# Kernel optimization log

Measured on AMD Instinct MI355X. Metric: run time of the kernel, lower is better.

Reference implementation:

```python
import jax, jax.numpy as jnp
import numpy as np

N = 50000      # nodes
E = 800000     # edges
XS = 64        # x_size
ES = 32        # edge_attr dim (in_size = XS + ES = 96)
OUT = 64       # out_size
H = 128        # hidden_size
EPS = 1e-5


def _lin_init(k, fan_in, fan_out):
    s = 1.0 / np.sqrt(fan_in)
    kw, kb = jax.random.split(k)
    w = jax.random.uniform(kw, (fan_in, fan_out), minval=-s, maxval=s, dtype=jnp.float32)
    b = jax.random.uniform(kb, (fan_out,), minval=-s, maxval=s, dtype=jnp.float32)
    return w, b


def setup_inputs() -> dict:
    key = jax.random.key(0)
    ks = jax.random.split(key, 12)
    x = jax.random.normal(ks[0], (N, XS), dtype=jnp.float32)
    edge_index = jax.random.randint(ks[1], (2, E), 0, N, dtype=jnp.int64)
    edge_attr = jax.random.normal(ks[2], (E, ES), dtype=jnp.float32)
    u = jax.random.normal(ks[3], (1, 8), dtype=jnp.float32)
    batch = jnp.zeros((N,), dtype=jnp.int64)
    # MLP1: (96->128) LReLU (128->128) LReLU (128->64) LReLU LN(64)
    m1w0, m1b0 = _lin_init(ks[4], XS + ES, H)
    m1w1, m1b1 = _lin_init(ks[5], H, H)
    m1w2, m1b2 = _lin_init(ks[6], H, OUT)
    ln1_g = jnp.ones((OUT,), jnp.float32); ln1_b = jnp.zeros((OUT,), jnp.float32)
    # MLP2: (128->128) LReLU (128->128) LReLU (128->64) LReLU LN(64)
    m2w0, m2b0 = _lin_init(ks[7], XS + OUT, H)
    m2w1, m2b1 = _lin_init(ks[8], H, H)
    m2w2, m2b2 = _lin_init(ks[9], H, OUT)
    ln2_g = jnp.ones((OUT,), jnp.float32); ln2_b = jnp.zeros((OUT,), jnp.float32)
    return dict(x=x, edge_index=edge_index, edge_attr=edge_attr, u=u, batch=batch,
                m1w0=m1w0, m1b0=m1b0, m1w1=m1w1, m1b1=m1b1, m1w2=m1w2, m1b2=m1b2,
                ln1_g=ln1_g, ln1_b=ln1_b,
                m2w0=m2w0, m2b0=m2b0, m2w1=m2w1, m2b1=m2b1, m2w2=m2w2, m2b2=m2b2,
                ln2_g=ln2_g, ln2_b=ln2_b)


def _lrelu(v):
    return jax.nn.leaky_relu(v, 0.01)


def _layernorm(v, g, b):
    mu = jnp.mean(v, axis=-1, keepdims=True)
    var = jnp.mean(jnp.square(v - mu), axis=-1, keepdims=True)
    return (v - mu) * jax.lax.rsqrt(var + EPS) * g + b


def _mlp(h, w0, b0, w1, b1, w2, b2, g, bn):
    h = _lrelu(h @ w0 + b0)
    h = _lrelu(h @ w1 + b1)
    h = _lrelu(h @ w2 + b2)          # activate_last=True
    return _layernorm(h, g, bn)      # layer_norm=True


def reference(x, edge_index, edge_attr, u, batch,
              m1w0, m1b0, m1w1, m1b1, m1w2, m1b2, ln1_g, ln1_b,
              m2w0, m2b0, m2w1, m2b1, m2w2, m2b2, ln2_g, ln2_b):
    row, col = edge_index[0], edge_index[1]
    # gather source nodes, concat edge features -> per-edge MLP
    h = jnp.concatenate([x[row], edge_attr], axis=1)            # [E, 96]
    h = _mlp(h, m1w0, m1b0, m1w1, m1b1, m1w2, m1b2, ln1_g, ln1_b)  # [E, 64]
    # scatter_mean over destination nodes
    agg = jax.ops.segment_sum(h, col, num_segments=N)           # [N, 64]
    cnt = jax.ops.segment_sum(jnp.ones((E,), h.dtype), col, num_segments=N)
    agg = agg / jnp.maximum(cnt, 1.0)[:, None]
    # node update MLP
    h2 = jnp.concatenate([x, agg], axis=1)                      # [N, 128]
    return _mlp(h2, m2w0, m2b0, m2w1, m2b1, m2w2, m2b2, ln2_g, ln2_b)
```

## Files before the change

### kernel.cpp

```cpp
#include <hip/hip_runtime.h>


#define NNODES 50000
#define NEDGES 800000

typedef __bf16 bf16;
typedef __bf16 __attribute__((ext_vector_type(4))) bf16x4;
typedef __bf16 __attribute__((ext_vector_type(8))) bf16x8;
typedef float __attribute__((ext_vector_type(4))) f32x4;

__device__ __forceinline__ f32x4 mfma_bf16(bf16x8 a, bf16x8 b, f32x4 c) {
    return __builtin_amdgcn_mfma_f32_16x16x32_bf16(a, b, c, 0, 0, 0);
}

__global__ void prep_weights(const float* __restrict__ w10, const float* __restrict__ w11,
                             const float* __restrict__ w12, const float* __restrict__ w20,
                             const float* __restrict__ w21, const float* __restrict__ w22,
                             bf16* __restrict__ img) {
    int idx = blockIdx.x * 256 + threadIdx.x;
    if (idx >= 77824) return;
    const float* w; int N; int t;
    if (idx < 12288)      { w = w10; N = 128; t = idx; }
    else if (idx < 28672) { w = w11; N = 128; t = idx - 12288; }
    else if (idx < 36864) { w = w12; N = 64;  t = idx - 28672; }
    else if (idx < 53248) { w = w20; N = 128; t = idx - 36864; }
    else if (idx < 69632) { w = w21; N = 128; t = idx - 53248; }
    else                  { w = w22; N = 64;  t = idx - 69632; }
    int j = t & 7, lane = (t >> 3) & 63, blk = t >> 9;
    int NT = N >> 4;
    int nt = blk % NT, ks = blk / NT;
    int k = ks * 32 + ((lane >> 4) << 3) + j;
    int n = nt * 16 + (lane & 15);
    img[idx] = (bf16)w[k * N + n];
}

__global__ void hist_kernel(const int* __restrict__ col, int* __restrict__ hist) {
    int i = blockIdx.x * 512 + threadIdx.x;
    if (i < NEDGES) atomicAdd(hist + col[i], 1);
}

__global__ void scanA(const int* __restrict__ hist, int* __restrict__ off,
                      int* __restrict__ csum) {
    __shared__ int sd[512];
    int t = threadIdx.x, i = blockIdx.x * 512 + t;
    int v = (i < NNODES) ? hist[i] : 0;
    sd[t] = v;
    __syncthreads();
    for (int o2 = 1; o2 < 512; o2 <<= 1) {
        int x = (t >= o2) ? sd[t - o2] : 0;
        __syncthreads();
        sd[t] += x;
        __syncthreads();
    }
    if (i < NNODES) off[i] = sd[t] - v;
    if (t == 511) csum[blockIdx.x] = sd[511];
}

__global__ void scanB(int* __restrict__ csum) {
    __shared__ int sd[128];
    int t = threadIdx.x;
    int v = (t < 98) ? csum[t] : 0;
    sd[t] = v;
    __syncthreads();
    for (int o2 = 1; o2 < 128; o2 <<= 1) {
        int x = (t >= o2) ? sd[t - o2] : 0;
        __syncthreads();
        sd[t] += x;
        __syncthreads();
    }
    if (t < 98) csum[t] = sd[t] - v;
}

__global__ void scanC(int* __restrict__ off, const int* __restrict__ csum) {
    int i = blockIdx.x * 512 + threadIdx.x;
    if (i < NNODES) off[i] += csum[blockIdx.x];
}

__global__ void scatter_kernel(const int* __restrict__ eidx, int* __restrict__ off,
                               int2* __restrict__ prd) {
    int i = blockIdx.x * 512 + threadIdx.x;
    if (i < NEDGES) {
        int r = eidx[i], d = eidx[NEDGES + i];
        int pos = atomicAdd(off + d, 1);
        prd[pos] = make_int2(i, r | (d << 16));
    }
}

__global__ __launch_bounds__(256, 2) void edge_mlp(
    const float* __restrict__ x, const int2* __restrict__ prd,
    const float* __restrict__ eattr, const bf16* __restrict__ wimg,
    const float* __restrict__ b0g, const float* __restrict__ b1g,
    const float* __restrict__ b2g, const float* __restrict__ lng,
    const float* __restrict__ lnb, float* __restrict__ agg) {
    __shared__ __align__(16) bf16 atile[128 * 104];
    __shared__ __align__(16) bf16 hid[128 * 136];

    const int tid = threadIdx.x;
    const int lane = tid & 63;
    const int wv = tid >> 6;
    const int col16 = lane & 15;
    const int quad = lane >> 4;

    float b0r[8], b1r[8], b2r[4], gr[4], br[4];
#pragma unroll
    for (int i = 0; i < 8; i++) { b0r[i] = b0g[i * 16 + col16]; b1r[i] = b1g[i * 16 + col16]; }
#pragma unroll
    for (int i = 0; i < 4; i++) {
        b2r[i] = b2g[i * 16 + col16];
        gr[i] = lng[i * 16 + col16];
        br[i] = lnb[i * 16 + col16];
    }

    const bf16* wl = wimg + (size_t)lane * 8;
    const f32x4 vzero = {0.0f, 0.0f, 0.0f, 0.0f};
    const int r0 = wv * 32 + col16;
    const int rw = wv * 32 + quad * 4;
    const int sbase = blockIdx.x * 128;

    int vreg;
    {
        const int el = tid >> 1, half = tid & 1;
        int2 v = prd[sbase + el];
        vreg = v.y;
        const int r = v.y & 0xFFFF;
        const float4* xs = (const float4*)(x + (size_t)r * 64);
        bf16* arow = atile + el * 104;
#pragma unroll
        for (int j = 0; j < 8; j++) {
            float4 vv = xs[half * 8 + j];
            bf16x4 u = {(bf16)vv.x, (bf16)vv.y, (bf16)vv.z, (bf16)vv.w};
            *(bf16x4*)(arow + half * 32 + j * 4) = u;
        }
        const float4* es = (const float4*)(eattr + (size_t)v.x * 32);
#pragma unroll
        for (int j = 0; j < 4; j++) {
            float4 vv = es[half * 4 + j];
            bf16x4 u = {(bf16)vv.x, (bf16)vv.y, (bf16)vv.z, (bf16)vv.w};
            *(bf16x4*)(arow + 64 + half * 16 + j * 4) = u;
        }
    }

    f32x4 acc1[2][8];
#pragma unroll
    for (int mt = 0; mt < 2; mt++)
#pragma unroll
        for (int nt = 0; nt < 8; nt++) acc1[mt][nt] = vzero;
#pragma unroll
    for (int ks = 0; ks < 3; ks++) {
        bf16x8 a0 = *(const bf16x8*)(atile + r0 * 104 + ks * 32 + quad * 8);
        bf16x8 a1 = *(const bf16x8*)(atile + (r0 + 16) * 104 + ks * 32 + quad * 8);
#pragma unroll
        for (int nt = 0; nt < 8; nt++) {
            bf16x8 b = *(const bf16x8*)(wl + (ks * 8 + nt) * 512);
            acc1[0][nt] = mfma_bf16(a0, b, acc1[0][nt]);
            acc1[1][nt] = mfma_bf16(a1, b, acc1[1][nt]);
        }
    }
#pragma unroll
    for (int mt = 0; mt < 2; mt++)
#pragma unroll
        for (int nt = 0; nt < 8; nt++)
#pragma unroll
            for (int rg = 0; rg < 4; rg++) {
                float v = acc1[mt][nt][rg] + b0r[nt];
                v = (v > 0.0f) ? v : 0.01f * v;
                hid[(rw + mt * 16 + rg) * 136 + nt * 16 + col16] = (bf16)v;
            }

    bf16x8 a2[2][4];
#pragma unroll
    for (int mt = 0; mt < 2; mt++)
#pragma unroll
        for (int ks = 0; ks < 4; ks++)
            a2[mt][ks] = *(const bf16x8*)(hid + (r0 + mt * 16) * 136 + ks * 32 + quad * 8);
    f32x4 acc2[2][8];
#pragma unroll
    for (int mt = 0; mt < 2; mt++)
#pragma unroll
        for (int nt = 0; nt < 8; nt++) acc2[mt][nt] = vzero;
#pragma unroll
    for (int ks = 0; ks < 4; ks++) {
#pragma unroll
        for (int nt = 0; nt < 8; nt++) {
            bf16x8 b = *(const bf16x8*)(wl + 12288 + (ks * 8 + nt) * 512);
            acc2[0][nt] = mfma_bf16(a2[0][ks], b, acc2[0][nt]);
            acc2[1][nt] = mfma_bf16(a2[1][ks], b, acc2[1][nt]);
        }
    }
#pragma unroll
    for (int mt = 0; mt < 2; mt++)
#pragma unroll
        for (int nt = 0; nt < 8; nt++)
#pragma unroll
            for (int rg = 0; rg < 4; rg++) {
                float v = acc2[mt][nt][rg] + b1r[nt];
                v = (v > 0.0f) ? v : 0.01f * v;
                hid[(rw + mt * 16 + rg) * 136 + nt * 16 + col16] = (bf16)v;
            }

    bf16x8 a3[2][4];
#pragma unroll
    for (int mt = 0; mt < 2; mt++)
#pragma unroll
        for (int ks = 0; ks < 4; ks++)
            a3[mt][ks] = *(const bf16x8*)(hid + (r0 + mt * 16) * 136 + ks * 32 + quad * 8);
    f32x4 acc3[2][4];
#pragma unroll
    for (int mt = 0; mt < 2; mt++)
#pragma unroll
        for (int nt = 0; nt < 4; nt++) acc3[mt][nt] = vzero;
#pragma unroll
    for (int ks = 0; ks < 4; ks++) {
#pragma unroll
        for (int nt = 0; nt < 4; nt++) {
            bf16x8 b = *(const bf16x8*)(wl + 28672 + (ks * 4 + nt) * 512);
            acc3[0][nt] = mfma_bf16(a3[0][ks], b, acc3[0][nt]);
            acc3[1][nt] = mfma_bf16(a3[1][ks], b, acc3[1][nt]);
        }
    }

#pragma unroll
    for (int mt = 0; mt < 2; mt++) {
        float vals[4][4];
        float s1[4] = {0.f, 0.f, 0.f, 0.f}, s2[4] = {0.f, 0.f, 0.f, 0.f};
#pragma unroll
        for (int nt = 0; nt < 4; nt++)
#pragma unroll
            for (int rg = 0; rg < 4; rg++) {
                float v = acc3[mt][nt][rg] + b2r[nt];
                v = (v > 0.0f) ? v : 0.01f * v;
                vals[nt][rg] = v;
                s1[rg] += v;
                s2[rg] += v * v;
            }
#pragma unroll
        for (int off2 = 1; off2 < 16; off2 <<= 1) {
#pragma unroll
            for (int rg = 0; rg < 4; rg++) {
                s1[rg] += __shfl_xor(s1[rg], off2);
                s2[rg] += __shfl_xor(s2[rg], off2);
            }
        }
        float o[4][4];
        int dr[4];
#pragma unroll
        for (int rg = 0; rg < 4; rg++) {
            float mu = s1[rg] * 0.015625f;
            float var = s2[rg] * 0.015625f - mu * mu;
            float rstd = rsqrtf(var + 1e-5f);
            dr[rg] = ((unsigned)__shfl(vreg, (mt * 16 + quad * 4 + rg) << 1)) >> 16;
#pragma unroll
            for (int nt = 0; nt < 4; nt++)
                o[nt][rg] = (vals[nt][rg] - mu) * rstd * gr[nt] + br[nt];
        }
        float run0 = o[0][0], run1 = o[1][0], run2 = o[2][0], run3 = o[3][0];
        int cur = dr[0];
#pragma unroll
        for (int rg = 1; rg < 4; rg++) {
            if (dr[rg] != cur) {
                float* dst = agg + (size_t)cur * 64 + col16;
                atomicAdd(dst, run0); atomicAdd(dst + 16, run1);
                atomicAdd(dst + 32, run2); atomicAdd(dst + 48, run3);
                run0 = o[0][rg]; run1 = o[1][rg]; run2 = o[2][rg]; run3 = o[3][rg];
                cur = dr[rg];
            } else {
                run0 += o[0][rg]; run1 += o[1][rg]; run2 += o[2][rg]; run3 += o[3][rg];
            }
        }
        float* dst = agg + (size_t)cur * 64 + col16;
        atomicAdd(dst, run0); atomicAdd(dst + 16, run1);
        atomicAdd(dst + 32, run2); atomicAdd(dst + 48, run3);
    }
}

__global__ __launch_bounds__(256, 2) void node_mlp(
    const float* __restrict__ x, const float* __restrict__ agg,
    const int* __restrict__ hist, const bf16* __restrict__ wimg,
    const float* __restrict__ b0g, const float* __restrict__ b1g,
    const float* __restrict__ b2g, const float* __restrict__ lng,
    const float* __restrict__ lnb, float* __restrict__ out) {
    __shared__ __align__(16) bf16 atile[128 * 136];
    __shared__ __align__(16) bf16 hid[128 * 136];

    const int tid = threadIdx.x;
    const int lane = tid & 63;
    const int wv = tid >> 6;
    const int col16 = lane & 15;
    const int quad = lane >> 4;

    float b0r[8], b1r[8], b2r[4], gr[4], br[4];
#pragma unroll
    for (int i = 0; i < 8; i++) { b0r[i] = b0g[i * 16 + col16]; b1r[i] = b1g[i * 16 + col16]; }
#pragma unroll
    for (int i = 0; i < 4; i++) {
        b2r[i] = b2g[i * 16 + col16];
        gr[i] = lng[i * 16 + col16];
        br[i] = lnb[i * 16 + col16];
    }

    const bf16* wl = wimg + 36864 + (size_t)lane * 8;
    const f32x4 vzero = {0.0f, 0.0f, 0.0f, 0.0f};
    const int r0 = wv * 32 + col16;
    const int rw = wv * 32 + quad * 4;
    const int nbase = blockIdx.x * 128;

    {
        const int el = tid >> 1, half = tid & 1;
        int i = nbase + el;
        if (i >= NNODES) i = NNODES - 1;
        const float4* xs = (const float4*)(x + (size_t)i * 64);
        bf16* arow = atile + el * 136;
#pragma unroll
        for (int j = 0; j < 8; j++) {
            float4 v = xs[half * 8 + j];
            bf16x4 u = {(bf16)v.x, (bf16)v.y, (bf16)v.z, (bf16)v.w};
            *(bf16x4*)(arow + half * 32 + j * 4) = u;
        }
        int c = hist[i];
        float inv = 1.0f / (float)(c > 1 ? c : 1);
        const float4* as = (const float4*)(agg + (size_t)i * 64);
#pragma unroll
        for (int j = 0; j < 8; j++) {
            float4 v = as[half * 8 + j];
            bf16x4 u = {(bf16)(v.x * inv), (bf16)(v.y * inv), (bf16)(v.z * inv), (bf16)(v.w * inv)};
            *(bf16x4*)(arow + 64 + half * 32 + j * 4) = u;
        }
    }

    f32x4 acc1[2][8];
#pragma unroll
    for (int mt = 0; mt < 2; mt++)
#pragma unroll
        for (int nt = 0; nt < 8; nt++) acc1[mt][nt] = vzero;
#pragma unroll
    for (int ks = 0; ks < 4; ks++) {
        bf16x8 a0 = *(const bf16x8*)(atile + r0 * 136 + ks * 32 + quad * 8);
        bf16x8 a1 = *(const bf16x8*)(atile + (r0 + 16) * 136 + ks * 32 + quad * 8);
#pragma unroll
        for (int nt = 0; nt < 8; nt++) {
            bf16x8 b = *(const bf16x8*)(wl + (ks * 8 + nt) * 512);
            acc1[0][nt] = mfma_bf16(a0, b, acc1[0][nt]);
            acc1[1][nt] = mfma_bf16(a1, b, acc1[1][nt]);
        }
    }
#pragma unroll
    for (int mt = 0; mt < 2; mt++)
#pragma unroll
        for (int nt = 0; nt < 8; nt++)
#pragma unroll
            for (int rg = 0; rg < 4; rg++) {
                float v = acc1[mt][nt][rg] + b0r[nt];
                v = (v > 0.0f) ? v : 0.01f * v;
                hid[(rw + mt * 16 + rg) * 136 + nt * 16 + col16] = (bf16)v;
            }

    bf16x8 a2[2][4];
#pragma unroll
    for (int mt = 0; mt < 2; mt++)
#pragma unroll
        for (int ks = 0; ks < 4; ks++)
            a2[mt][ks] = *(const bf16x8*)(hid + (r0 + mt * 16) * 136 + ks * 32 + quad * 8);
    f32x4 acc2[2][8];
#pragma unroll
    for (int mt = 0; mt < 2; mt++)
#pragma unroll
        for (int nt = 0; nt < 8; nt++) acc2[mt][nt] = vzero;
#pragma unroll
    for (int ks = 0; ks < 4; ks++) {
#pragma unroll
        for (int nt = 0; nt < 8; nt++) {
            bf16x8 b = *(const bf16x8*)(wl + 16384 + (ks * 8 + nt) * 512);
            acc2[0][nt] = mfma_bf16(a2[0][ks], b, acc2[0][nt]);
            acc2[1][nt] = mfma_bf16(a2[1][ks], b, acc2[1][nt]);
        }
    }
#pragma unroll
    for (int mt = 0; mt < 2; mt++)
#pragma unroll
        for (int nt = 0; nt < 8; nt++)
#pragma unroll
            for (int rg = 0; rg < 4; rg++) {
                float v = acc2[mt][nt][rg] + b1r[nt];
                v = (v > 0.0f) ? v : 0.01f * v;
                hid[(rw + mt * 16 + rg) * 136 + nt * 16 + col16] = (bf16)v;
            }

    bf16x8 a3[2][4];
#pragma unroll
    for (int mt = 0; mt < 2; mt++)
#pragma unroll
        for (int ks = 0; ks < 4; ks++)
            a3[mt][ks] = *(const bf16x8*)(hid + (r0 + mt * 16) * 136 + ks * 32 + quad * 8);
    f32x4 acc3[2][4];
#pragma unroll
    for (int mt = 0; mt < 2; mt++)
#pragma unroll
        for (int nt = 0; nt < 4; nt++) acc3[mt][nt] = vzero;
#pragma unroll
    for (int ks = 0; ks < 4; ks++) {
#pragma unroll
        for (int nt = 0; nt < 4; nt++) {
            bf16x8 b = *(const bf16x8*)(wl + 32768 + (ks * 4 + nt) * 512);
            acc3[0][nt] = mfma_bf16(a3[0][ks], b, acc3[0][nt]);
            acc3[1][nt] = mfma_bf16(a3[1][ks], b, acc3[1][nt]);
        }
    }

#pragma unroll
    for (int mt = 0; mt < 2; mt++) {
        float vals[4][4];
        float s1[4] = {0.f, 0.f, 0.f, 0.f}, s2[4] = {0.f, 0.f, 0.f, 0.f};
#pragma unroll
        for (int nt = 0; nt < 4; nt++)
#pragma unroll
            for (int rg = 0; rg < 4; rg++) {
                float v = acc3[mt][nt][rg] + b2r[nt];
                v = (v > 0.0f) ? v : 0.01f * v;
                vals[nt][rg] = v;
                s1[rg] += v;
                s2[rg] += v * v;
            }
#pragma unroll
        for (int off2 = 1; off2 < 16; off2 <<= 1) {
#pragma unroll
            for (int rg = 0; rg < 4; rg++) {
                s1[rg] += __shfl_xor(s1[rg], off2);
                s2[rg] += __shfl_xor(s2[rg], off2);
            }
        }
#pragma unroll
        for (int rg = 0; rg < 4; rg++) {
            float mu = s1[rg] * 0.015625f;
            float var = s2[rg] * 0.015625f - mu * mu;
            float rstd = rsqrtf(var + 1e-5f);
            int i = nbase + rw + mt * 16 + rg;
            if (i < NNODES) {
#pragma unroll
                for (int nt = 0; nt < 4; nt++) {
                    float o = (vals[nt][rg] - mu) * rstd * gr[nt] + br[nt];
                    out[(size_t)i * 64 + nt * 16 + col16] = o;
                }
            }
        }
    }
}

extern "C" void kernel_launch(void* const* d_in, const int* in_sizes, int n_in,
                              void* d_out, int out_size, void* d_ws, size_t ws_size,
                              hipStream_t stream) {
    (void)in_sizes; (void)n_in; (void)out_size; (void)ws_size;
    const float* x     = (const float*)d_in[0];
    const int*   eidx  = (const int*)d_in[1];
    const float* eattr = (const float*)d_in[2];
    const float* m1w0 = (const float*)d_in[5];
    const float* m1b0 = (const float*)d_in[6];
    const float* m1w1 = (const float*)d_in[7];
    const float* m1b1 = (const float*)d_in[8];
    const float* m1w2 = (const float*)d_in[9];
    const float* m1b2 = (const float*)d_in[10];
    const float* ln1g = (const float*)d_in[11];
    const float* ln1b = (const float*)d_in[12];
    const float* m2w0 = (const float*)d_in[13];
    const float* m2b0 = (const float*)d_in[14];
    const float* m2w1 = (const float*)d_in[15];
    const float* m2b1 = (const float*)d_in[16];
    const float* m2w2 = (const float*)d_in[17];
    const float* m2b2 = (const float*)d_in[18];
    const float* ln2g = (const float*)d_in[19];
    const float* ln2b = (const float*)d_in[20];

    char* ws = (char*)d_ws;
    float* agg  = (float*)ws;
    int*   hist = (int*)(ws + 12800000);
    int*   off  = (int*)(ws + 13000000);
    int*   csum = (int*)(ws + 13200000);
    int2*  prd  = (int2*)(ws + 13200512);
    bf16*  wimg = (bf16*)(ws + 19600512);

    hipMemsetAsync(d_ws, 0, 13000000, stream);
    prep_weights<<<304, 256, 0, stream>>>(m1w0, m1w1, m1w2, m2w0, m2w1, m2w2, wimg);
    hist_kernel<<<1563, 512, 0, stream>>>(eidx + NEDGES, hist);
    scanA<<<98, 512, 0, stream>>>(hist, off, csum);
    scanB<<<1, 128, 0, stream>>>(csum);
    scanC<<<98, 512, 0, stream>>>(off, csum);
    scatter_kernel<<<1563, 512, 0, stream>>>(eidx, off, prd);
    edge_mlp<<<6250, 256, 0, stream>>>(x, prd, eattr, wimg, m1b0, m1b1, m1b2,
                                       ln1g, ln1b, agg);
    node_mlp<<<391, 256, 0, stream>>>(x, agg, hist, wimg,
                                      m2b0, m2b1, m2b2, ln2g, ln2b, (float*)d_out);
}
```

Before: 558.9 us.

## Fold scan fixup into scatter and shrink node MLP blocks to one wave

Drops the separate scanC kernel launch. The scatter kernel now adds the per-block scan prefix (csum[d>>9]) itself when it computes each edge's slot. The node MLP is restructured from 256-thread, 128-row blocks to single-wave, 32-row blocks. Each lane loads its x and agg fragments straight into MFMA A-operand registers instead of staging them through a shared tile. This removes one launch, cuts shared memory, and spreads the node stage over more blocks, at the cost of extra csum reads in the scatter and more weight fetches per node row.

```diff
diff --git a/kernel.cpp b/kernel.cpp
--- a/kernel.cpp
+++ b/kernel.cpp
@@ -11,6 +11,13 @@
 
 __device__ __forceinline__ f32x4 mfma_bf16(bf16x8 a, bf16x8 b, f32x4 c) {
     return __builtin_amdgcn_mfma_f32_16x16x32_bf16(a, b, c, 0, 0, 0);
+}
+
+__device__ __forceinline__ bf16x8 pack8(float4 a, float4 b) {
+    bf16x8 r;
+    r[0] = (bf16)a.x; r[1] = (bf16)a.y; r[2] = (bf16)a.z; r[3] = (bf16)a.w;
+    r[4] = (bf16)b.x; r[5] = (bf16)b.y; r[6] = (bf16)b.z; r[7] = (bf16)b.w;
+    return r;
 }
 
 __global__ void prep_weights(const float* __restrict__ w10, const float* __restrict__ w11,
@@ -71,17 +78,12 @@
     if (t < 98) csum[t] = sd[t] - v;
 }
 
-__global__ void scanC(int* __restrict__ off, const int* __restrict__ csum) {
-    int i = blockIdx.x * 512 + threadIdx.x;
-    if (i < NNODES) off[i] += csum[blockIdx.x];
-}
-
 __global__ void scatter_kernel(const int* __restrict__ eidx, int* __restrict__ off,
-                               int2* __restrict__ prd) {
+                               const int* __restrict__ csum, int2* __restrict__ prd) {
     int i = blockIdx.x * 512 + threadIdx.x;
     if (i < NEDGES) {
         int r = eidx[i], d = eidx[NEDGES + i];
-        int pos = atomicAdd(off + d, 1);
+        int pos = atomicAdd(off + d, 1) + csum[d >> 9];
         prd[pos] = make_int2(i, r | (d << 16));
     }
 }
@@ -273,18 +275,15 @@
     }
 }
 
-__global__ __launch_bounds__(256, 2) void node_mlp(
+__global__ __launch_bounds__(64, 4) void node_mlp(
     const float* __restrict__ x, const float* __restrict__ agg,
     const int* __restrict__ hist, const bf16* __restrict__ wimg,
     const float* __restrict__ b0g, const float* __restrict__ b1g,
     const float* __restrict__ b2g, const float* __restrict__ lng,
     const float* __restrict__ lnb, float* __restrict__ out) {
-    __shared__ __align__(16) bf16 atile[128 * 136];
-    __shared__ __align__(16) bf16 hid[128 * 136];
-
-    const int tid = threadIdx.x;
-    const int lane = tid & 63;
-    const int wv = tid >> 6;
+    __shared__ __align__(16) bf16 hid[32 * 136];
+
+    const int lane = threadIdx.x;
     const int col16 = lane & 15;
     const int quad = lane >> 4;
 
@@ -300,31 +299,29 @@
 
     const bf16* wl = wimg + 36864 + (size_t)lane * 8;
     const f32x4 vzero = {0.0f, 0.0f, 0.0f, 0.0f};
-    const int r0 = wv * 32 + col16;
-    const int rw = wv * 32 + quad * 4;
-    const int nbase = blockIdx.x * 128;
-
-    {
-        const int el = tid >> 1, half = tid & 1;
-        int i = nbase + el;
+    const int nbase = blockIdx.x * 32;
+
+    bf16x8 a1[2][4];
+#pragma unroll
+    for (int mt = 0; mt < 2; mt++) {
+        int i = nbase + col16 + 16 * mt;
         if (i >= NNODES) i = NNODES - 1;
-        const float4* xs = (const float4*)(x + (size_t)i * 64);
-        bf16* arow = atile + el * 136;
-#pragma unroll
-        for (int j = 0; j < 8; j++) {
-            float4 v = xs[half * 8 + j];
-            bf16x4 u = {(bf16)v.x, (bf16)v.y, (bf16)v.z, (bf16)v.w};
-            *(bf16x4*)(arow + half * 32 + j * 4) = u;
-        }
+        const float4* xr = (const float4*)(x + (size_t)i * 64);
+        float4 x0 = xr[quad * 2], x1 = xr[quad * 2 + 1];
+        float4 x2 = xr[8 + quad * 2], x3 = xr[8 + quad * 2 + 1];
         int c = hist[i];
         float inv = 1.0f / (float)(c > 1 ? c : 1);
-        const float4* as = (const float4*)(agg + (size_t)i * 64);
-#pragma unroll
-        for (int j = 0; j < 8; j++) {
-            float4 v = as[half * 8 + j];
-            bf16x4 u = {(bf16)(v.x * inv), (bf16)(v.y * inv), (bf16)(v.z * inv), (bf16)(v.w * inv)};
-            *(bf16x4*)(arow + 64 + half * 32 + j * 4) = u;
-        }
+        const float4* ar = (const float4*)(agg + (size_t)i * 64);
+        float4 g0 = ar[quad * 2], g1 = ar[quad * 2 + 1];
+        float4 g2 = ar[8 + quad * 2], g3 = ar[8 + quad * 2 + 1];
+        a1[mt][0] = pack8(x0, x1);
+        a1[mt][1] = pack8(x2, x3);
+        float4 h0 = {g0.x * inv, g0.y * inv, g0.z * inv, g0.w * inv};
+        float4 h1 = {g1.x * inv, g1.y * inv, g1.z * inv, g1.w * inv};
+        float4 h2 = {g2.x * inv, g2.y * inv, g2.z * inv, g2.w * inv};
+        float4 h3 = {g3.x * inv, g3.y * inv, g3.z * inv, g3.w * inv};
+        a1[mt][2] = pack8(h0, h1);
+        a1[mt][3] = pack8(h2, h3);
     }
 
     f32x4 acc1[2][8];
@@ -334,15 +331,14 @@
         for (int nt = 0; nt < 8; nt++) acc1[mt][nt] = vzero;
 #pragma unroll
     for (int ks = 0; ks < 4; ks++) {
-        bf16x8 a0 = *(const bf16x8*)(atile + r0 * 136 + ks * 32 + quad * 8);
-        bf16x8 a1 = *(const bf16x8*)(atile + (r0 + 16) * 136 + ks * 32 + quad * 8);
 #pragma unroll
         for (int nt = 0; nt < 8; nt++) {
             bf16x8 b = *(const bf16x8*)(wl + (ks * 8 + nt) * 512);
-            acc1[0][nt] = mfma_bf16(a0, b, acc1[0][nt]);
-            acc1[1][nt] = mfma_bf16(a1, b, acc1[1][nt]);
-        }
-    }
+            acc1[0][nt] = mfma_bf16(a1[0][ks], b, acc1[0][nt]);
+            acc1[1][nt] = mfma_bf16(a1[1][ks], b, acc1[1][nt]);
+        }
+    }
+    const int rw = quad * 4;
 #pragma unroll
     for (int mt = 0; mt < 2; mt++)
 #pragma unroll
@@ -359,7 +355,7 @@
     for (int mt = 0; mt < 2; mt++)
 #pragma unroll
         for (int ks = 0; ks < 4; ks++)
-            a2[mt][ks] = *(const bf16x8*)(hid + (r0 + mt * 16) * 136 + ks * 32 + quad * 8);
+            a2[mt][ks] = *(const bf16x8*)(hid + (col16 + 16 * mt) * 136 + ks * 32 + quad * 8);
     f32x4 acc2[2][8];
 #pragma unroll
     for (int mt = 0; mt < 2; mt++)
@@ -390,7 +386,7 @@
     for (int mt = 0; mt < 2; mt++)
 #pragma unroll
         for (int ks = 0; ks < 4; ks++)
-            a3[mt][ks] = *(const bf16x8*)(hid + (r0 + mt * 16) * 136 + ks * 32 + quad * 8);
+            a3[mt][ks] = *(const bf16x8*)(hid + (col16 + 16 * mt) * 136 + ks * 32 + quad * 8);
     f32x4 acc3[2][4];
 #pragma unroll
     for (int mt = 0; mt < 2; mt++)
@@ -433,7 +429,7 @@
             float mu = s1[rg] * 0.015625f;
             float var = s2[rg] * 0.015625f - mu * mu;
             float rstd = rsqrtf(var + 1e-5f);
-            int i = nbase + rw + mt * 16 + rg;
+            int i = nbase + mt * 16 + quad * 4 + rg;
             if (i < NNODES) {
 #pragma unroll
                 for (int nt = 0; nt < 4; nt++) {
@@ -482,10 +478,9 @@
     hist_kernel<<<1563, 512, 0, stream>>>(eidx + NEDGES, hist);
     scanA<<<98, 512, 0, stream>>>(hist, off, csum);
     scanB<<<1, 128, 0, stream>>>(csum);
-    scanC<<<98, 512, 0, stream>>>(off, csum);
-    scatter_kernel<<<1563, 512, 0, stream>>>(eidx, off, prd);
+    scatter_kernel<<<1563, 512, 0, stream>>>(eidx, off, csum, prd);
     edge_mlp<<<6250, 256, 0, stream>>>(x, prd, eattr, wimg, m1b0, m1b1, m1b2,
                                        ln1g, ln1b, agg);
-    node_mlp<<<391, 256, 0, stream>>>(x, agg, hist, wimg,
+    node_mlp<<<1563, 64, 0, stream>>>(x, agg, hist, wimg,
                                       m2b0, m2b1, m2b2, ln2g, ln2b, (float*)d_out);
 }
```

After: 552.1 us. About the same (-1.2%).
